# Kernel tuning notes

Measured on AMD Instinct MI355X. Metric: run time of the kernel, lower is better.

## Reference

```python
import math
import itertools
import jax, jax.numpy as jnp
import numpy as np

QUALITY = 95
FACTOR = (200.0 - 2.0 * QUALITY) / 100.0  # quality>=50 branch -> 0.1

# ---- constant tables (match original torch Parameters) ----
_Y = np.array([
    [16, 11, 10, 16, 24, 40, 51, 61],
    [12, 12, 14, 19, 26, 58, 60, 55],
    [14, 13, 16, 24, 40, 57, 69, 56],
    [14, 17, 22, 29, 51, 87, 80, 62],
    [18, 22, 37, 56, 68, 109, 103, 77],
    [24, 35, 55, 64, 81, 104, 113, 92],
    [49, 64, 78, 87, 103, 121, 120, 101],
    [72, 92, 95, 98, 112, 100, 103, 99]], dtype=np.float32)
Y_TABLE = jnp.asarray(_Y.T)
_C = np.full((8, 8), 99.0, dtype=np.float32)
_C[:4, :4] = np.array([[17, 18, 24, 47], [18, 21, 26, 66],
                       [24, 26, 56, 99], [47, 66, 99, 99]], dtype=np.float32).T
C_TABLE = jnp.asarray(_C)

RGB2YCBCR = jnp.asarray(np.array([
    [0.299, 0.587, 0.114],
    [-0.168736, -0.331264, 0.5],
    [0.5, -0.418688, -0.081312]], dtype=np.float32))
YCBCR2RGB = jnp.asarray(np.array([
    [1.0, 0.0, 1.402],
    [1.0, -0.344136, -0.714136],
    [1.0, 1.772, 0.0]], dtype=np.float32))

_cosmat = np.cos((2 * np.arange(8)[:, None] + 1) * np.arange(8)[None, :] * np.pi / 16).astype(np.float32)  # [x,u]
DCT_T = jnp.asarray(np.einsum('xu,yv->xyuv', _cosmat, _cosmat))   # tensor[x,y,u,v]
IDCT_T = jnp.asarray(np.einsum('ux,vy->xyuv', _cosmat, _cosmat))  # cos((2u+1)x..)cos((2v+1)y..)
_alpha = np.array([1.0 / np.sqrt(2)] + [1.0] * 7, dtype=np.float32)
ALPHA = jnp.asarray(np.outer(_alpha, _alpha))
DCT_SCALE = ALPHA * 0.25


def diff_round(x):
    s = jnp.zeros_like(x)
    for n in range(1, 10):
        s = s + ((-1.0) ** (n + 1) / n) * jnp.sin(2.0 * math.pi * n * x)
    return x - s / math.pi


def _avgpool2(x):  # [B,H,W] -> [B,H/2,W/2]
    b, h, w = x.shape
    return x.reshape(b, h // 2, 2, w // 2, 2).mean(axis=(2, 4))


def _block_split(x):  # [B,H,W] -> [B,N,8,8]
    b, h, w = x.shape
    return x.reshape(b, h // 8, 8, w // 8, 8).transpose(0, 1, 3, 2, 4).reshape(b, -1, 8, 8)


def _block_merge(p, h, w):  # [B,N,8,8] -> [B,h,w]
    b = p.shape[0]
    return p.reshape(b, h // 8, w // 8, 8, 8).transpose(0, 1, 3, 2, 4).reshape(b, h, w)


def _compress_component(comp, table):
    blocks = _block_split(comp) - 128.0
    dct = DCT_SCALE * jnp.einsum('bnxy,xyuv->bnuv', blocks, DCT_T)
    return diff_round(dct / (table * FACTOR))


def _decompress_component(q, table, h, w):
    d = q * (table * FACTOR)
    idct = 0.25 * jnp.einsum('bnxy,xyuv->bnuv', d * ALPHA, IDCT_T) + 128.0
    return _block_merge(idct, h, w)


def _diffjpeg(x):
    b, c, h, w = x.shape
    img = x * 255.0
    # RGB -> YCbCr (pixel @ RGB2YCBCR.T) + shift
    ycbcr = jnp.einsum('bchw,oc->bhwo', img, RGB2YCBCR) + jnp.array([0.0, 128.0, 128.0], dtype=x.dtype)
    y = ycbcr[..., 0]
    cb = _avgpool2(ycbcr[..., 1])
    cr = _avgpool2(ycbcr[..., 2])
    # compress
    yq = _compress_component(y, Y_TABLE)
    cbq = _compress_component(cb, C_TABLE)
    crq = _compress_component(cr, C_TABLE)
    # decompress
    y2 = _decompress_component(yq, Y_TABLE, h, w)
    cb2 = _decompress_component(cbq, C_TABLE, h // 2, w // 2)
    cr2 = _decompress_component(crq, C_TABLE, h // 2, w // 2)
    cb_up = jnp.repeat(jnp.repeat(cb2, 2, axis=1), 2, axis=2)
    cr_up = jnp.repeat(jnp.repeat(cr2, 2, axis=1), 2, axis=2)
    ycc = jnp.stack([y2, cb_up, cr_up], axis=3)  # [B,H,W,3]
    rgb = jnp.einsum('bhwc,oc->bhwo', ycc + jnp.array([0.0, -128.0, -128.0], dtype=x.dtype), YCBCR2RGB)
    rgb = rgb.transpose(0, 3, 1, 2)  # [B,3,H,W]
    rgb = jnp.clip(rgb, 0.0, 255.0)
    return rgb / 255.0


def setup_inputs() -> dict:
    key = jax.random.key(0)
    x = jax.random.uniform(key, (16, 3, 512, 512), dtype=jnp.float32)
    return {"x": x}


def reference(x):
    return _diffjpeg(x)
```

## Files before the change

### kernel.cpp

```cpp
#include <hip/hip_runtime.h>


__device__ constexpr float YTAB8[8][8] = {
    {16, 12, 14, 14, 18, 24, 49, 72},
    {11, 12, 13, 17, 22, 35, 64, 92},
    {10, 14, 16, 22, 37, 55, 78, 95},
    {16, 19, 24, 29, 56, 64, 87, 98},
    {24, 26, 40, 51, 68, 81, 103, 112},
    {40, 58, 57, 87, 109, 104, 121, 100},
    {51, 60, 69, 80, 103, 113, 120, 103},
    {61, 55, 56, 62, 77, 92, 101, 99}};

__device__ constexpr float CTAB8[8][8] = {
    {17, 18, 24, 47, 99, 99, 99, 99},
    {18, 21, 26, 66, 99, 99, 99, 99},
    {24, 26, 56, 99, 99, 99, 99, 99},
    {47, 66, 99, 99, 99, 99, 99, 99},
    {99, 99, 99, 99, 99, 99, 99, 99},
    {99, 99, 99, 99, 99, 99, 99, 99},
    {99, 99, 99, 99, 99, 99, 99, 99},
    {99, 99, 99, 99, 99, 99, 99, 99}};

#define C1f 0.9807852804032304f
#define C2f 0.9238795325112867f
#define C3f 0.8314696123025452f
#define C4f 0.7071067811865476f
#define C5f 0.5555702330196022f
#define C6f 0.3826834323650898f
#define C7f 0.1950903220161283f

__device__ __forceinline__ void dct8(float y[8]) {
    float e0=y[0]+y[7], e1=y[1]+y[6], e2=y[2]+y[5], e3=y[3]+y[4];
    float o0=y[0]-y[7], o1=y[1]-y[6], o2=y[2]-y[5], o3=y[3]-y[4];
    float t0=e0+e3, t1=e1+e2, d0=e0-e3, d1=e1-e2;
    y[0]=t0+t1; y[4]=(t0-t1)*C4f;
    y[2]=d0*C2f+d1*C6f; y[6]=d0*C6f-d1*C2f;
    y[1]=o0*C1f+o1*C3f+o2*C5f+o3*C7f;
    y[3]=o0*C3f-o1*C7f-o2*C1f-o3*C5f;
    y[5]=o0*C5f-o1*C1f+o2*C7f+o3*C3f;
    y[7]=o0*C7f-o1*C5f+o2*C3f-o3*C1f;
}

__device__ __forceinline__ void idct8(float y[8]) {
    float a=y[4]*C4f, p=y[0]+a, m=y[0]-a;
    float q=y[2]*C2f+y[6]*C6f, w=y[2]*C6f-y[6]*C2f;
    float E0=p+q, E1=m+w, E2=m-w, E3=p-q;
    float O0=y[1]*C1f+y[3]*C3f+y[5]*C5f+y[7]*C7f;
    float O1=y[1]*C3f-y[3]*C7f-y[5]*C1f-y[7]*C5f;
    float O2=y[1]*C5f-y[3]*C1f+y[5]*C7f+y[7]*C3f;
    float O3=y[1]*C7f-y[3]*C5f+y[5]*C3f-y[7]*C1f;
    y[0]=E0+O0; y[7]=E0-O0; y[1]=E1+O1; y[6]=E1-O1;
    y[2]=E2+O2; y[5]=E2-O2; y[3]=E3+O3; y[4]=E3-O3;
}

__device__ __forceinline__ void transpose8(float y[8]) {
    const int lane = threadIdx.x & 63;
#pragma unroll
    for (int s = 1; s <= 4; s <<= 1) {
        const bool upper = (lane & (s << 3)) != 0;
#pragma unroll
        for (int j = 0; j < 8; ++j) {
            if ((j & s) == 0) {
                float a = y[j], b2 = y[j | s];
                float t = upper ? a : b2;
                t = __shfl_xor(t, s << 3, 64);
                if (upper) y[j] = t; else y[j | s] = t;
            }
        }
    }
}

__device__ __forceinline__ void wave_lds_fence() {
    __builtin_amdgcn_wave_barrier();
    asm volatile("s_waitcnt lgkmcnt(0)" ::: "memory");
    __builtin_amdgcn_wave_barrier();
}

__device__ __forceinline__ float diff_round_f(float x) {
    float f = __builtin_amdgcn_fractf(x);
    float sc = __builtin_amdgcn_sinf(f);
    float c1v = __builtin_amdgcn_cosf(f);
    float twoc = 2.0f * c1v;
    float sp = 0.0f, acc = 0.0f;
    const float coef[9] = {1.0f, -0.5f, 1.0f/3.0f, -0.25f, 0.2f,
                           -1.0f/6.0f, 1.0f/7.0f, -0.125f, 1.0f/9.0f};
#pragma unroll
    for (int n = 0; n < 9; ++n) {
        acc += coef[n] * sc;
        float sn = twoc * sc - sp;
        sp = sc; sc = sn;
    }
    return x - acc * 0.3183098861837907f;
}

__device__ __forceinline__ void jpeg_block(float y[8], const float* qs, int r) {
    dct8(y); transpose8(y); dct8(y);
#pragma unroll
    for (int j = 0; j < 8; ++j) {
        float s1v = qs[2 * (j * 8 + r)];
        float s2v = qs[2 * (j * 8 + r) + 1];
        y[j] = diff_round_f(y[j] * s1v) * s2v;
    }
    idct8(y); transpose8(y); idct8(y);
}

__global__ __launch_bounds__(128, 6) void diffjpeg_kernel(
        const float* __restrict__ x, float* __restrict__ out) {
    __shared__ float QS[2][128];
    __shared__ float PL[2][2][8][17];
    __shared__ float CL[2][2][8][17];

    const int tid = threadIdx.x;

    {
        int type = tid >> 6;
        int k = tid & 63, u = k >> 3, v = k & 7;
        float t = (type ? CTAB8[u][v] : YTAB8[u][v]) * 0.1f;
        float aa = 0.25f * ((u == 0) ? C4f : 1.0f) * ((v == 0) ? C4f : 1.0f);
        QS[type][2 * k]     = aa / t;
        QS[type][2 * k + 1] = aa * t;
    }
    __syncthreads();

    const int wv = tid >> 6;
    const int lane = tid & 63;
    const int r = lane >> 3;
    const int b = lane & 7;

    const int img = blockIdx.y;
    const int strip = blockIdx.x * 2 + wv;
    const int sy = (strip >> 4) * 16;
    const int sx = (strip & 15) * 32;
    const size_t plane = (size_t)512 * 512;
    const float* src = x + (size_t)img * 3 * plane;
    float* dst = out + (size_t)img * 3 * plane;

    const int br = b >> 2, bc = b & 3;
    const int py = sy + br * 8 + r;
    const int px = sx + bc * 8;

    float y[8];
    {
        const float* p = src + (size_t)py * 512 + px;
        float4 R0 = *(const float4*)(p);
        float4 R1 = *(const float4*)(p + 4);
        float4 G0 = *(const float4*)(p + plane);
        float4 G1 = *(const float4*)(p + plane + 4);
        float4 B0 = *(const float4*)(p + 2 * plane);
        float4 B1 = *(const float4*)(p + 2 * plane + 4);
        y[0] = 76.245f*R0.x + 149.685f*G0.x + 29.07f*B0.x - 128.0f;
        y[1] = 76.245f*R0.y + 149.685f*G0.y + 29.07f*B0.y - 128.0f;
        y[2] = 76.245f*R0.z + 149.685f*G0.z + 29.07f*B0.z - 128.0f;
        y[3] = 76.245f*R0.w + 149.685f*G0.w + 29.07f*B0.w - 128.0f;
        y[4] = 76.245f*R1.x + 149.685f*G1.x + 29.07f*B1.x - 128.0f;
        y[5] = 76.245f*R1.y + 149.685f*G1.y + 29.07f*B1.y - 128.0f;
        y[6] = 76.245f*R1.z + 149.685f*G1.z + 29.07f*B1.z - 128.0f;
        y[7] = 76.245f*R1.w + 149.685f*G1.w + 29.07f*B1.w - 128.0f;
        float rh0=R0.x+R0.y, rh1=R0.z+R0.w, rh2=R1.x+R1.y, rh3=R1.z+R1.w;
        float gh0=G0.x+G0.y, gh1=G0.z+G0.w, gh2=G1.x+G1.y, gh3=G1.z+G1.w;
        float bh0=B0.x+B0.y, bh1=B0.z+B0.w, bh2=B1.x+B1.y, bh3=B1.z+B1.w;
        const float kbr = -10.75692f, kbg = -21.11808f, kbb = 31.875f;
        const float krr =  31.875f,   krg = -26.69136f, krb = -5.18364f;
        float cb[4], cr[4];
        cb[0]=kbr*rh0+kbg*gh0+kbb*bh0; cb[1]=kbr*rh1+kbg*gh1+kbb*bh1;
        cb[2]=kbr*rh2+kbg*gh2+kbb*bh2; cb[3]=kbr*rh3+kbg*gh3+kbb*bh3;
        cr[0]=krr*rh0+krg*gh0+krb*bh0; cr[1]=krr*rh1+krg*gh1+krb*bh1;
        cr[2]=krr*rh2+krg*gh2+krb*bh2; cr[3]=krr*rh3+krg*gh3+krb*bh3;
#pragma unroll
        for (int k = 0; k < 4; ++k) {
            cb[k] += __shfl_xor(cb[k], 8, 64);
            cr[k] += __shfl_xor(cr[k], 8, 64);
        }
        if (!(r & 1)) {
            const int prow = br * 4 + (r >> 1);
            const int pc = bc * 4;
#pragma unroll
            for (int k = 0; k < 4; ++k) {
                PL[wv][0][prow][pc + k] = cb[k];
                PL[wv][1][prow][pc + k] = cr[k];
            }
        }
    }
    wave_lds_fence();

    jpeg_block(y, QS[0], r);

    {
        const int ch = (b >> 1) & 1;
        const int cblk = b & 1;
        float c[8];
#pragma unroll
        for (int j = 0; j < 8; ++j) c[j] = PL[wv][ch][r][cblk * 8 + j];
        jpeg_block(c, QS[1], r);
        if (b < 4) {
#pragma unroll
            for (int j = 0; j < 8; ++j) CL[wv][ch][r][cblk * 8 + j] = c[j];
        }
    }
    wave_lds_fence();

    {
        const int prow = br * 4 + (r >> 1);
        const int pc = bc * 4;
        float cbv[4], crv[4];
#pragma unroll
        for (int jj = 0; jj < 4; ++jj) {
            cbv[jj] = CL[wv][0][prow][pc + jj];
            crv[jj] = CL[wv][1][prow][pc + jj];
        }
        float* p = dst + (size_t)py * 512 + px;
        float o[8];
#pragma unroll
        for (int j = 0; j < 8; ++j) {
            float v = (y[j] + 128.0f) + 1.402f * crv[j >> 1];
            o[j] = fminf(fmaxf(v, 0.0f), 255.0f) * (1.0f / 255.0f);
        }
        *(float4*)(p)     = make_float4(o[0], o[1], o[2], o[3]);
        *(float4*)(p + 4) = make_float4(o[4], o[5], o[6], o[7]);
#pragma unroll
        for (int j = 0; j < 8; ++j) {
            float v = (y[j] + 128.0f) - 0.344136f * cbv[j >> 1] - 0.714136f * crv[j >> 1];
            o[j] = fminf(fmaxf(v, 0.0f), 255.0f) * (1.0f / 255.0f);
        }
        *(float4*)(p + plane)     = make_float4(o[0], o[1], o[2], o[3]);
        *(float4*)(p + plane + 4) = make_float4(o[4], o[5], o[6], o[7]);
#pragma unroll
        for (int j = 0; j < 8; ++j) {
            float v = (y[j] + 128.0f) + 1.772f * cbv[j >> 1];
            o[j] = fminf(fmaxf(v, 0.0f), 255.0f) * (1.0f / 255.0f);
        }
        *(float4*)(p + 2 * plane)     = make_float4(o[0], o[1], o[2], o[3]);
        *(float4*)(p + 2 * plane + 4) = make_float4(o[4], o[5], o[6], o[7]);
    }
}

extern "C" void kernel_launch(void* const* d_in, const int* in_sizes, int n_in,
                              void* d_out, int out_size, void* d_ws, size_t ws_size,
                              hipStream_t stream) {
    const float* x = (const float*)d_in[0];
    float* out = (float*)d_out;
    dim3 grid(256, 16);
    dim3 block(128);
    diffjpeg_kernel<<<grid, block, 0, stream>>>(x, out);
}
```

Baseline: 24.23 us.

## Process two strips per wave with prefetch of second strip during first compute

Each wave now handles two 16x32 strips instead of one, halving the grid to 2048 blocks. The second strip's global loads are issued before the first strip's DCT/quantize work so memory latency overlaps compute. Launch bounds occupancy hint drops from 6 to 4 to leave room for the extra live registers. This trades occupancy-based latency hiding for explicit software prefetch.

```diff
diff --git a/kernel.cpp b/kernel.cpp
--- a/kernel.cpp
+++ b/kernel.cpp
@@ -104,14 +104,121 @@
     idct8(y); transpose8(y); idct8(y);
 }
 
-__global__ __launch_bounds__(128, 6) void diffjpeg_kernel(
+struct Raw { float4 R0, R1, G0, G1, B0, B1; };
+
+#define PLANE ((size_t)512 * 512)
+
+__device__ __forceinline__ Raw issue_load(const float* __restrict__ src,
+                                          int py, int px) {
+    const float* p = src + (size_t)py * 512 + px;
+    Raw L;
+    L.R0 = *(const float4*)(p);
+    L.R1 = *(const float4*)(p + 4);
+    L.G0 = *(const float4*)(p + PLANE);
+    L.G1 = *(const float4*)(p + PLANE + 4);
+    L.B0 = *(const float4*)(p + 2 * PLANE);
+    L.B1 = *(const float4*)(p + 2 * PLANE + 4);
+    return L;
+}
+
+__device__ __forceinline__ void convert_pool(const Raw& L, float y[8],
+                                             float cb[4], float cr[4]) {
+    y[0] = 76.245f*L.R0.x + 149.685f*L.G0.x + 29.07f*L.B0.x - 128.0f;
+    y[1] = 76.245f*L.R0.y + 149.685f*L.G0.y + 29.07f*L.B0.y - 128.0f;
+    y[2] = 76.245f*L.R0.z + 149.685f*L.G0.z + 29.07f*L.B0.z - 128.0f;
+    y[3] = 76.245f*L.R0.w + 149.685f*L.G0.w + 29.07f*L.B0.w - 128.0f;
+    y[4] = 76.245f*L.R1.x + 149.685f*L.G1.x + 29.07f*L.B1.x - 128.0f;
+    y[5] = 76.245f*L.R1.y + 149.685f*L.G1.y + 29.07f*L.B1.y - 128.0f;
+    y[6] = 76.245f*L.R1.z + 149.685f*L.G1.z + 29.07f*L.B1.z - 128.0f;
+    y[7] = 76.245f*L.R1.w + 149.685f*L.G1.w + 29.07f*L.B1.w - 128.0f;
+    float rh0=L.R0.x+L.R0.y, rh1=L.R0.z+L.R0.w, rh2=L.R1.x+L.R1.y, rh3=L.R1.z+L.R1.w;
+    float gh0=L.G0.x+L.G0.y, gh1=L.G0.z+L.G0.w, gh2=L.G1.x+L.G1.y, gh3=L.G1.z+L.G1.w;
+    float bh0=L.B0.x+L.B0.y, bh1=L.B0.z+L.B0.w, bh2=L.B1.x+L.B1.y, bh3=L.B1.z+L.B1.w;
+    const float kbr = -10.75692f, kbg = -21.11808f, kbb = 31.875f;
+    const float krr =  31.875f,   krg = -26.69136f, krb = -5.18364f;
+    cb[0]=kbr*rh0+kbg*gh0+kbb*bh0; cb[1]=kbr*rh1+kbg*gh1+kbb*bh1;
+    cb[2]=kbr*rh2+kbg*gh2+kbb*bh2; cb[3]=kbr*rh3+kbg*gh3+kbb*bh3;
+    cr[0]=krr*rh0+krg*gh0+krb*bh0; cr[1]=krr*rh1+krg*gh1+krb*bh1;
+    cr[2]=krr*rh2+krg*gh2+krb*bh2; cr[3]=krr*rh3+krg*gh3+krb*bh3;
+#pragma unroll
+    for (int k = 0; k < 4; ++k) {
+        cb[k] += __shfl_xor(cb[k], 8, 64);
+        cr[k] += __shfl_xor(cr[k], 8, 64);
+    }
+}
+
+__device__ __forceinline__ void process_store(
+        float y[8], const float cb[4], const float cr[4],
+        float* __restrict__ dst, int py, int px,
+        const float (*QS)[128], float (*PL)[8][17], float (*CL)[8][17],
+        int r, int b, int br, int bc) {
+    if (!(r & 1)) {
+        const int prow = br * 4 + (r >> 1);
+        const int pc = bc * 4;
+#pragma unroll
+        for (int k = 0; k < 4; ++k) {
+            PL[0][prow][pc + k] = cb[k];
+            PL[1][prow][pc + k] = cr[k];
+        }
+    }
+    wave_lds_fence();
+
+    jpeg_block(y, QS[0], r);
+
+    {
+        const int ch = (b >> 1) & 1;
+        const int cblk = b & 1;
+        float c[8];
+#pragma unroll
+        for (int j = 0; j < 8; ++j) c[j] = PL[ch][r][cblk * 8 + j];
+        jpeg_block(c, QS[1], r);
+        if (b < 4) {
+#pragma unroll
+            for (int j = 0; j < 8; ++j) CL[ch][r][cblk * 8 + j] = c[j];
+        }
+    }
+    wave_lds_fence();
+
+    const int prow = br * 4 + (r >> 1);
+    const int pc = bc * 4;
+    float cbv[4], crv[4];
+#pragma unroll
+    for (int jj = 0; jj < 4; ++jj) {
+        cbv[jj] = CL[0][prow][pc + jj];
+        crv[jj] = CL[1][prow][pc + jj];
+    }
+    float* p = dst + (size_t)py * 512 + px;
+    float o[8];
+#pragma unroll
+    for (int j = 0; j < 8; ++j) {
+        float v = (y[j] + 128.0f) + 1.402f * crv[j >> 1];
+        o[j] = fminf(fmaxf(v, 0.0f), 255.0f) * (1.0f / 255.0f);
+    }
+    *(float4*)(p)     = make_float4(o[0], o[1], o[2], o[3]);
+    *(float4*)(p + 4) = make_float4(o[4], o[5], o[6], o[7]);
+#pragma unroll
+    for (int j = 0; j < 8; ++j) {
+        float v = (y[j] + 128.0f) - 0.344136f * cbv[j >> 1] - 0.714136f * crv[j >> 1];
+        o[j] = fminf(fmaxf(v, 0.0f), 255.0f) * (1.0f / 255.0f);
+    }
+    *(float4*)(p + PLANE)     = make_float4(o[0], o[1], o[2], o[3]);
+    *(float4*)(p + PLANE + 4) = make_float4(o[4], o[5], o[6], o[7]);
+#pragma unroll
+    for (int j = 0; j < 8; ++j) {
+        float v = (y[j] + 128.0f) + 1.772f * cbv[j >> 1];
+        o[j] = fminf(fmaxf(v, 0.0f), 255.0f) * (1.0f / 255.0f);
+    }
+    *(float4*)(p + 2 * PLANE)     = make_float4(o[0], o[1], o[2], o[3]);
+    *(float4*)(p + 2 * PLANE + 4) = make_float4(o[4], o[5], o[6], o[7]);
+}
+
+__global__ __launch_bounds__(128, 4) void diffjpeg_kernel(
         const float* __restrict__ x, float* __restrict__ out) {
     __shared__ float QS[2][128];
-    __shared__ float PL[2][2][8][17];
-    __shared__ float CL[2][2][8][17];
+    __shared__ float PLs[2][2][8][17];
+    __shared__ float CLs[2][2][8][17];
 
     const int tid = threadIdx.x;
-
     {
         int type = tid >> 6;
         int k = tid & 63, u = k >> 3, v = k & 7;
@@ -126,112 +233,37 @@
     const int lane = tid & 63;
     const int r = lane >> 3;
     const int b = lane & 7;
-
-    const int img = blockIdx.y;
-    const int strip = blockIdx.x * 2 + wv;
-    const int sy = (strip >> 4) * 16;
-    const int sx = (strip & 15) * 32;
-    const size_t plane = (size_t)512 * 512;
-    const float* src = x + (size_t)img * 3 * plane;
-    float* dst = out + (size_t)img * 3 * plane;
-
     const int br = b >> 2, bc = b & 3;
-    const int py = sy + br * 8 + r;
-    const int px = sx + bc * 8;
-
-    float y[8];
-    {
-        const float* p = src + (size_t)py * 512 + px;
-        float4 R0 = *(const float4*)(p);
-        float4 R1 = *(const float4*)(p + 4);
-        float4 G0 = *(const float4*)(p + plane);
-        float4 G1 = *(const float4*)(p + plane + 4);
-        float4 B0 = *(const float4*)(p + 2 * plane);
-        float4 B1 = *(const float4*)(p + 2 * plane + 4);
-        y[0] = 76.245f*R0.x + 149.685f*G0.x + 29.07f*B0.x - 128.0f;
-        y[1] = 76.245f*R0.y + 149.685f*G0.y + 29.07f*B0.y - 128.0f;
-        y[2] = 76.245f*R0.z + 149.685f*G0.z + 29.07f*B0.z - 128.0f;
-        y[3] = 76.245f*R0.w + 149.685f*G0.w + 29.07f*B0.w - 128.0f;
-        y[4] = 76.245f*R1.x + 149.685f*G1.x + 29.07f*B1.x - 128.0f;
-        y[5] = 76.245f*R1.y + 149.685f*G1.y + 29.07f*B1.y - 128.0f;
-        y[6] = 76.245f*R1.z + 149.685f*G1.z + 29.07f*B1.z - 128.0f;
-        y[7] = 76.245f*R1.w + 149.685f*G1.w + 29.07f*B1.w - 128.0f;
-        float rh0=R0.x+R0.y, rh1=R0.z+R0.w, rh2=R1.x+R1.y, rh3=R1.z+R1.w;
-        float gh0=G0.x+G0.y, gh1=G0.z+G0.w, gh2=G1.x+G1.y, gh3=G1.z+G1.w;
-        float bh0=B0.x+B0.y, bh1=B0.z+B0.w, bh2=B1.x+B1.y, bh3=B1.z+B1.w;
-        const float kbr = -10.75692f, kbg = -21.11808f, kbb = 31.875f;
-        const float krr =  31.875f,   krg = -26.69136f, krb = -5.18364f;
-        float cb[4], cr[4];
-        cb[0]=kbr*rh0+kbg*gh0+kbb*bh0; cb[1]=kbr*rh1+kbg*gh1+kbb*bh1;
-        cb[2]=kbr*rh2+kbg*gh2+kbb*bh2; cb[3]=kbr*rh3+kbg*gh3+kbb*bh3;
-        cr[0]=krr*rh0+krg*gh0+krb*bh0; cr[1]=krr*rh1+krg*gh1+krb*bh1;
-        cr[2]=krr*rh2+krg*gh2+krb*bh2; cr[3]=krr*rh3+krg*gh3+krb*bh3;
-#pragma unroll
-        for (int k = 0; k < 4; ++k) {
-            cb[k] += __shfl_xor(cb[k], 8, 64);
-            cr[k] += __shfl_xor(cr[k], 8, 64);
-        }
-        if (!(r & 1)) {
-            const int prow = br * 4 + (r >> 1);
-            const int pc = bc * 4;
-#pragma unroll
-            for (int k = 0; k < 4; ++k) {
-                PL[wv][0][prow][pc + k] = cb[k];
-                PL[wv][1][prow][pc + k] = cr[k];
-            }
-        }
-    }
-    wave_lds_fence();
-
-    jpeg_block(y, QS[0], r);
-
-    {
-        const int ch = (b >> 1) & 1;
-        const int cblk = b & 1;
-        float c[8];
-#pragma unroll
-        for (int j = 0; j < 8; ++j) c[j] = PL[wv][ch][r][cblk * 8 + j];
-        jpeg_block(c, QS[1], r);
-        if (b < 4) {
-#pragma unroll
-            for (int j = 0; j < 8; ++j) CL[wv][ch][r][cblk * 8 + j] = c[j];
-        }
-    }
-    wave_lds_fence();
-
-    {
-        const int prow = br * 4 + (r >> 1);
-        const int pc = bc * 4;
-        float cbv[4], crv[4];
-#pragma unroll
-        for (int jj = 0; jj < 4; ++jj) {
-            cbv[jj] = CL[wv][0][prow][pc + jj];
-            crv[jj] = CL[wv][1][prow][pc + jj];
-        }
-        float* p = dst + (size_t)py * 512 + px;
-        float o[8];
-#pragma unroll
-        for (int j = 0; j < 8; ++j) {
-            float v = (y[j] + 128.0f) + 1.402f * crv[j >> 1];
-            o[j] = fminf(fmaxf(v, 0.0f), 255.0f) * (1.0f / 255.0f);
-        }
-        *(float4*)(p)     = make_float4(o[0], o[1], o[2], o[3]);
-        *(float4*)(p + 4) = make_float4(o[4], o[5], o[6], o[7]);
-#pragma unroll
-        for (int j = 0; j < 8; ++j) {
-            float v = (y[j] + 128.0f) - 0.344136f * cbv[j >> 1] - 0.714136f * crv[j >> 1];
-            o[j] = fminf(fmaxf(v, 0.0f), 255.0f) * (1.0f / 255.0f);
-        }
-        *(float4*)(p + plane)     = make_float4(o[0], o[1], o[2], o[3]);
-        *(float4*)(p + plane + 4) = make_float4(o[4], o[5], o[6], o[7]);
-#pragma unroll
-        for (int j = 0; j < 8; ++j) {
-            float v = (y[j] + 128.0f) + 1.772f * cbv[j >> 1];
-            o[j] = fminf(fmaxf(v, 0.0f), 255.0f) * (1.0f / 255.0f);
-        }
-        *(float4*)(p + 2 * plane)     = make_float4(o[0], o[1], o[2], o[3]);
-        *(float4*)(p + 2 * plane + 4) = make_float4(o[4], o[5], o[6], o[7]);
-    }
+
+    const int wave_gid = blockIdx.x * 2 + wv;
+
+    const int sid0 = wave_gid;
+    const int img0 = sid0 >> 9, loc0 = sid0 & 511;
+    const int py0 = (loc0 >> 4) * 16 + br * 8 + r;
+    const int px0 = (loc0 & 15) * 32 + bc * 8;
+    const float* src0 = x + (size_t)img0 * 3 * PLANE;
+
+    const int sid1 = wave_gid + 4096;
+    const int img1 = sid1 >> 9, loc1 = sid1 & 511;
+    const int py1 = (loc1 >> 4) * 16 + br * 8 + r;
+    const int px1 = (loc1 & 15) * 32 + bc * 8;
+    const float* src1 = x + (size_t)img1 * 3 * PLANE;
+
+    Raw L0 = issue_load(src0, py0, px0);
+
+    float y0[8], cb0[4], cr0[4];
+    convert_pool(L0, y0, cb0, cr0);
+
+    Raw L1 = issue_load(src1, py1, px1);
+
+    process_store(y0, cb0, cr0, out + (size_t)img0 * 3 * PLANE, py0, px0,
+                  QS, PLs[wv], CLs[wv], r, b, br, bc);
+
+    float y1[8], cb1[4], cr1[4];
+    convert_pool(L1, y1, cb1, cr1);
+
+    process_store(y1, cb1, cr1, out + (size_t)img1 * 3 * PLANE, py1, px1,
+                  QS, PLs[wv], CLs[wv], r, b, br, bc);
 }
 
 extern "C" void kernel_launch(void* const* d_in, const int* in_sizes, int n_in,
@@ -239,7 +271,7 @@
                               hipStream_t stream) {
     const float* x = (const float*)d_in[0];
     float* out = (float*)d_out;
-    dim3 grid(256, 16);
+    dim3 grid(2048);
     dim3 block(128);
     diffjpeg_kernel<<<grid, block, 0, stream>>>(x, out);
 }
```

Result: slower. 25.74 us (+6.2%).
